# Performance work log

Hardware: AMD Instinct MI355X
Metric: run time of the kernel (lower is better)

## Reference

```python
import math
import jax, jax.numpy as jnp
import numpy as np

B, T, D, S = 4, 8192, 1024, 32  # batch, seq, dim, num_slots; segment L = T // S


def setup_inputs() -> dict:
    key = jax.random.key(0)
    ks = jax.random.split(key, 11)
    d_inv_sqrt = D ** -0.5
    return {
        "x": jax.random.normal(ks[0], (B, T, D), jnp.float32),
        "gate_w": jax.random.normal(ks[1], (D, D), jnp.float32) * d_inv_sqrt,
        "gate_b": jnp.zeros((D,), jnp.float32),
        "read_q_w": jax.random.normal(ks[2], (D, D), jnp.float32) * 0.02,
        "read_k_w": jax.random.normal(ks[3], (D, D), jnp.float32) * 0.02,
        "read_v_w": jax.random.normal(ks[4], (D, D), jnp.float32) * 0.02,
        "output_w": jax.random.normal(ks[5], (D, D), jnp.float32) * d_inv_sqrt,
        "memory_slots": jax.random.normal(ks[6], (S, D), jnp.float32) * 0.02,
        "write_q_w": jax.random.normal(ks[7], (D, D), jnp.float32) * 0.02,
        "write_k_w": jax.random.normal(ks[8], (D, D), jnp.float32) * 0.02,
        "write_v_w": jax.random.normal(ks[9], (D, D), jnp.float32) * 0.02,
    }


def reference(x, gate_w, gate_b, read_q_w, read_k_w, read_v_w, output_w,
              memory_slots, write_q_w, write_k_w, write_v_w):
    b, t, d = x.shape
    s = memory_slots.shape[0]
    L = t // s  # segment length
    scale = 1.0 / math.sqrt(d)

    h = x @ gate_w.T + gate_b  # [B,T,D] gate pre-activation

    # --- write: per-slot attention over that slot's segment (block-diagonal) ---
    q = memory_slots @ write_q_w.T                      # [S,D]
    xs = x.reshape(b, s, L, d)                          # [B,S,L,D]
    k = xs @ write_k_w.T                                # [B,S,L,D]
    v = xs @ write_v_w.T                                # [B,S,L,D]
    wqk = jnp.einsum('sd,bsld->bsl', q, k) * scale      # [B,S,L]
    wattn = jax.nn.softmax(wqk, axis=-1)
    memory = jnp.einsum('bsl,bsld->bsd', wattn, v)      # [B,S,D]

    # --- read: masked cross-attention from tokens to memory slots ---
    rq = x @ read_q_w.T                                 # [B,T,D]
    rk = memory @ read_k_w.T                            # [B,S,D]
    rv = memory @ read_v_w.T                            # [B,S,D]
    rqk = jnp.einsum('btd,bsd->bts', rq, rk) * scale    # [B,T,S]
    seg = jnp.arange(t) // L                            # token -> segment index
    mask = seg[:, None] <= jnp.arange(s)[None, :]       # [T,S]; attend to slots >= own segment
    rqk = jnp.where(mask[None, :, :], rqk, -jnp.inf)
    rattn = jax.nn.softmax(rqk, axis=-1)
    read = jnp.einsum('bts,bsd->btd', rattn, rv)        # [B,T,D]

    y = x + jax.nn.sigmoid(h) * read
    out = y @ output_w.T
    return out, memory
```

## Files before the change

### kernel.cpp

```cpp
#include <hip/hip_runtime.h>
#include <stdint.h>

#define TB 4
#define TT 8192
#define TD 1024
#define TS 32
#define TL 256
#define BT 32768

typedef unsigned short u16;
typedef __bf16 bf16x8 __attribute__((ext_vector_type(8)));
typedef float f32x4 __attribute__((ext_vector_type(4)));

typedef uint32_t u32_g __attribute__((address_space(1)));
typedef uint32_t u32_l __attribute__((address_space(3)));

#define VMWAIT(N) asm volatile("s_waitcnt vmcnt(" #N ")" ::: "memory")
#define LGKM0()   asm volatile("s_waitcnt lgkmcnt(0)" ::: "memory")

__device__ __forceinline__ u16 f2b(float f){
  union { float f; uint32_t u; } a; a.f = f;
  uint32_t r = a.u + 0x7FFFu + ((a.u >> 16) & 1u);
  return (u16)(r >> 16);
}
__device__ __forceinline__ float b2f(u16 u){
  union { uint32_t u; float f; } a; a.u = ((uint32_t)u) << 16;
  return a.f;
}
__device__ __forceinline__ void gll16(const void* g, void* l){
  __builtin_amdgcn_global_load_lds((const u32_g*)g, (u32_l*)l, 16, 0, 0);
}

__global__ void k_tran(const float* __restrict__ w0, const float* __restrict__ w1,
                       const float* __restrict__ w2, const float* __restrict__ w3,
                       const float* __restrict__ w4, const float* __restrict__ ms,
                       u16* __restrict__ t0, u16* __restrict__ t1,
                       u16* __restrict__ t2, u16* __restrict__ t3,
                       u16* __restrict__ t4, u16* __restrict__ msb){
  int tid = threadIdx.x, z = blockIdx.z;
  if (z == 5){
    int i = (blockIdx.y*16 + blockIdx.x)*256 + tid;
    if (i < 8192){
      float4 v = ((const float4*)ms)[i];
      ushort4 u; u.x=f2b(v.x); u.y=f2b(v.y); u.z=f2b(v.z); u.w=f2b(v.w);
      ((ushort4*)msb)[i] = u;
    }
    return;
  }
  const float* src = (z==0)?w0:(z==1)?w1:(z==2)?w2:(z==3)?w3:w4;
  u16* dst = (z==0)?t0:(z==1)?t1:(z==2)?t2:(z==3)?t3:t4;
  __shared__ float sT[64][65];
  int r0 = blockIdx.y*64, c0 = blockIdx.x*64;
  int lr = tid >> 2, lc = (tid & 3)*16;
  #pragma unroll
  for (int j=0; j<4; ++j){
    float4 v = *(const float4*)(src + (size_t)(r0+lr)*TD + c0 + lc + j*4);
    sT[lr][lc+j*4+0]=v.x; sT[lr][lc+j*4+1]=v.y; sT[lr][lc+j*4+2]=v.z; sT[lr][lc+j*4+3]=v.w;
  }
  __syncthreads();
  int oc = tid >> 2, orh = (tid & 3)*16;
  #pragma unroll
  for (int j=0; j<4; ++j){
    ushort4 u;
    u.x = f2b(sT[orh+j*4+0][oc]);
    u.y = f2b(sT[orh+j*4+1][oc]);
    u.z = f2b(sT[orh+j*4+2][oc]);
    u.w = f2b(sT[orh+j*4+3][oc]);
    *(ushort4*)(dst + (size_t)(c0+oc)*TD + r0 + orh + j*4) = u;
  }
}

__global__ __launch_bounds__(512) void k_smmw(
    const u16* __restrict__ A0, const u16* __restrict__ W0, u16* __restrict__ O0, int tr0, float s0,
    const u16* __restrict__ A1, const u16* __restrict__ W1, u16* __restrict__ O1, int tr1, float s1){
  const u16 *A, *W; u16* O; int tr; float sc;
  if (blockIdx.z == 0){ A=A0; W=W0; O=O0; tr=tr0; sc=s0; }
  else                { A=A1; W=W1; O=O1; tr=tr1; sc=s1; }
  int tid = threadIdx.x, lane = tid & 63, wv = tid >> 6;
  int r15 = lane & 15, kg = lane >> 4;
  int wr = wv >> 2, wc = wv & 3;
  int m0 = blockIdx.y*128 + wr*64;
  int n0 = blockIdx.x*128 + wc*32;
  const u16* ap = A + (size_t)(m0 + r15)*TD + kg*8;
  const u16* bp = W + (size_t)(n0 + r15)*TD + kg*8;
  f32x4 acc[4][2];
  #pragma unroll
  for (int i=0;i<4;i++){ f32x4 z={0,0,0,0}; acc[i][0]=z; acc[i][1]=z; }
  #pragma unroll 2
  for (int k0=0; k0<TD; k0+=32){
    bf16x8 b0 = *(const bf16x8*)(bp + k0);
    bf16x8 b1 = *(const bf16x8*)(bp + 16*TD + k0);
    bf16x8 a0 = *(const bf16x8*)(ap + k0);
    bf16x8 a1 = *(const bf16x8*)(ap + 16*TD + k0);
    bf16x8 a2 = *(const bf16x8*)(ap + 32*TD + k0);
    bf16x8 a3 = *(const bf16x8*)(ap + 48*TD + k0);
    acc[0][0] = __builtin_amdgcn_mfma_f32_16x16x32_bf16(a0, b0, acc[0][0], 0,0,0);
    acc[0][1] = __builtin_amdgcn_mfma_f32_16x16x32_bf16(a0, b1, acc[0][1], 0,0,0);
    acc[1][0] = __builtin_amdgcn_mfma_f32_16x16x32_bf16(a1, b0, acc[1][0], 0,0,0);
    acc[1][1] = __builtin_amdgcn_mfma_f32_16x16x32_bf16(a1, b1, acc[1][1], 0,0,0);
    acc[2][0] = __builtin_amdgcn_mfma_f32_16x16x32_bf16(a2, b0, acc[2][0], 0,0,0);
    acc[2][1] = __builtin_amdgcn_mfma_f32_16x16x32_bf16(a2, b1, acc[2][1], 0,0,0);
    acc[3][0] = __builtin_amdgcn_mfma_f32_16x16x32_bf16(a3, b0, acc[3][0], 0,0,0);
    acc[3][1] = __builtin_amdgcn_mfma_f32_16x16x32_bf16(a3, b1, acc[3][1], 0,0,0);
  }
  #pragma unroll
  for (int mf=0; mf<4; ++mf){
    #pragma unroll
    for (int nf=0; nf<2; ++nf){
      int n = n0 + nf*16 + r15;
      #pragma unroll
      for (int qq=0; qq<4; ++qq){
        float v = acc[mf][nf][qq]*sc;
        int m = m0 + mf*16 + kg*4 + qq;
        if (tr) O[(size_t)n*TD + m] = f2b(v);
        else    O[(size_t)m*TD + n] = f2b(v);
      }
    }
  }
}

__global__ __launch_bounds__(512) void k_qk32(const u16* __restrict__ msb, const u16* __restrict__ WzT,
                                              float* __restrict__ qkp){
  int tid = threadIdx.x, lane = tid & 63, wv = tid >> 6;
  int r15 = lane & 15, kg = lane >> 4;
  int n0 = blockIdx.x*128 + wv*16;
  int kbase = blockIdx.y*512;
  const u16* ap = msb + (size_t)r15*TD + kbase + kg*8;
  const u16* bp = WzT + (size_t)(n0 + r15)*TD + kbase + kg*8;
  f32x4 a0 = {0,0,0,0}, a1 = {0,0,0,0};
  #pragma unroll 4
  for (int k0=0; k0<512; k0+=32){
    bf16x8 b  = *(const bf16x8*)(bp + k0);
    bf16x8 x0 = *(const bf16x8*)(ap + k0);
    bf16x8 x1 = *(const bf16x8*)(ap + 16*TD + k0);
    a0 = __builtin_amdgcn_mfma_f32_16x16x32_bf16(x0, b, a0, 0,0,0);
    a1 = __builtin_amdgcn_mfma_f32_16x16x32_bf16(x1, b, a1, 0,0,0);
  }
  const float sc = 1.0f/32.0f;
  float* o = qkp + (size_t)blockIdx.y*32768;
  #pragma unroll
  for (int qq=0; qq<4; ++qq){
    o[(size_t)(kg*4 + qq)*TD + n0 + r15]      = a0[qq]*sc;
    o[(size_t)(16 + kg*4 + qq)*TD + n0 + r15] = a1[qq]*sc;
  }
}

__global__ void k_convdot(const float* __restrict__ x, const float* __restrict__ qkp,
                          u16* __restrict__ xb, float* __restrict__ wqk,
                          const float* __restrict__ s0, const float* __restrict__ s1,
                          const float* __restrict__ s2, const float* __restrict__ s3,
                          const float* __restrict__ s4,
                          u16* __restrict__ d0, u16* __restrict__ d1,
                          u16* __restrict__ d2, u16* __restrict__ d3,
                          u16* __restrict__ d4){
  int tid = threadIdx.x;
  if (blockIdx.x >= 2048){
    int i = (blockIdx.x - 2048)*256 + tid;
    int mi = i >> 18, j = i & 262143;
    const float* src; u16* dst;
    if      (mi == 0){ src = s0; dst = d0; }
    else if (mi == 1){ src = s1; dst = d1; }
    else if (mi == 2){ src = s2; dst = d2; }
    else if (mi == 3){ src = s3; dst = d3; }
    else             { src = s4; dst = d4; }
    float4 v = ((const float4*)src)[j];
    ushort4 u; u.x=f2b(v.x); u.y=f2b(v.y); u.z=f2b(v.z); u.w=f2b(v.w);
    ((ushort4*)dst)[j] = u;
    return;
  }
  int lane = tid & 63, wv = tid >> 6;
  long bt0 = (long)blockIdx.x * 16;
  int sseg = (int)((bt0 & (TT-1)) >> 8);
  float qv[16];
  #pragma unroll
  for (int i=0;i<4;i++){
    const float* qp = qkp + (size_t)sseg*TD + i*256 + lane*4;
    float4 ta = *(const float4*)qp;
    float4 tb = *(const float4*)(qp + 32768);
    qv[i*4+0]=ta.x+tb.x; qv[i*4+1]=ta.y+tb.y; qv[i*4+2]=ta.z+tb.z; qv[i*4+3]=ta.w+tb.w;
  }
  for (int tok = wv; tok < 16; tok += 4){
    long bt = bt0 + tok;
    const float* xr = x + bt*TD;
    float dot = 0.f;
    #pragma unroll
    for (int i=0;i<4;i++){
      float4 t = *(const float4*)(xr + i*256 + lane*4);
      ushort4 u; u.x=f2b(t.x); u.y=f2b(t.y); u.z=f2b(t.z); u.w=f2b(t.w);
      *(ushort4*)(xb + bt*TD + i*256 + lane*4) = u;
      dot += t.x*qv[i*4] + t.y*qv[i*4+1] + t.z*qv[i*4+2] + t.w*qv[i*4+3];
    }
    #pragma unroll
    for (int o=32;o;o>>=1) dot += __shfl_xor(dot, o);
    if (lane == 0) wqk[bt] = dot;
  }
}

__global__ __launch_bounds__(512) void k_wattn_smm(
    const float* __restrict__ wqk, const u16* __restrict__ xb, u16* __restrict__ xbarb,
    const u16* __restrict__ A1, const u16* __restrict__ W1, u16* __restrict__ O1,
    const u16* __restrict__ A2, const u16* __restrict__ W2, u16* __restrict__ O2){
  __shared__ float sw[2][TL];
  __shared__ float red[2][8];
  __shared__ f32x4 part[2][4][64];
  int tid = threadIdx.x;
  if (blockIdx.x < 256){
    int u = tid >> 8;
    int unit = blockIdx.x*2 + u;
    int bs = unit >> 2, dch = unit & 3;
    int b = bs >> 5, s = bs & 31;
    int t2 = tid & 255, lane = t2 & 63, wv = t2 >> 6;
    long base = (long)b*TT + (long)s*TL;
    float v = wqk[base + t2];
    float m = v;
    #pragma unroll
    for (int o=32;o;o>>=1) m = fmaxf(m, __shfl_xor(m, o));
    if (lane == 0) red[u][wv] = m;
    __syncthreads();
    m = fmaxf(fmaxf(red[u][0], red[u][1]), fmaxf(red[u][2], red[u][3]));
    float e = __expf(v - m);
    float sm = e;
    #pragma unroll
    for (int o=32;o;o>>=1) sm += __shfl_xor(sm, o);
    if (lane == 0) red[u][4+wv] = sm;
    __syncthreads();
    sm = red[u][4]+red[u][5]+red[u][6]+red[u][7];
    sw[u][t2] = e / sm;
    __syncthreads();
    int d = dch*256 + lane*4;
    const u16* xp = xb + (base + wv*64)*TD + d;
    f32x4 acc = {0,0,0,0};
    #pragma unroll 8
    for (int i=0; i<64; ++i){
      float w = sw[u][wv*64 + i];
      ushort4 uu = *(const ushort4*)(xp + (size_t)i*TD);
      acc[0] += w*b2f(uu.x); acc[1] += w*b2f(uu.y); acc[2] += w*b2f(uu.z); acc[3] += w*b2f(uu.w);
    }
    part[u][wv][lane] = acc;
    __syncthreads();
    if (wv == 0){
      f32x4 t0 = part[u][0][lane], t1 = part[u][1][lane], t2v = part[u][2][lane], t3 = part[u][3][lane];
      ushort4 o;
      o.x = f2b(t0[0]+t1[0]+t2v[0]+t3[0]);
      o.y = f2b(t0[1]+t1[1]+t2v[1]+t3[1]);
      o.z = f2b(t0[2]+t1[2]+t2v[2]+t3[2]);
      o.w = f2b(t0[3]+t1[3]+t2v[3]+t3[3]);
      *(ushort4*)(xbarb + ((size_t)b*TS + s)*TD + d) = o;
    }
    return;
  }
  int bi = blockIdx.x - 256;
  const u16 *A, *W; u16* O; int tr;
  if (bi < 64){ A=A1; W=W1; O=O1; tr=0; }
  else        { A=A2; W=W2; O=O2; tr=1; bi -= 64; }
  int by = bi >> 3, bx = bi & 7;
  int lane = tid & 63, wv = tid >> 6;
  int r15 = lane & 15, kg = lane >> 4;
  int wr = wv >> 2, wc = wv & 3;
  int m0 = by*128 + wr*64;
  int n0 = bx*128 + wc*32;
  const u16* ap = A + (size_t)(m0 + r15)*TD + kg*8;
  const u16* bp = W + (size_t)(n0 + r15)*TD + kg*8;
  f32x4 acc[4][2];
  #pragma unroll
  for (int i=0;i<4;i++){ f32x4 z={0,0,0,0}; acc[i][0]=z; acc[i][1]=z; }
  #pragma unroll 2
  for (int k0=0; k0<TD; k0+=32){
    bf16x8 b0 = *(const bf16x8*)(bp + k0);
    bf16x8 b1 = *(const bf16x8*)(bp + 16*TD + k0);
    bf16x8 a0 = *(const bf16x8*)(ap + k0);
    bf16x8 a1 = *(const bf16x8*)(ap + 16*TD + k0);
    bf16x8 a2 = *(const bf16x8*)(ap + 32*TD + k0);
    bf16x8 a3 = *(const bf16x8*)(ap + 48*TD + k0);
    acc[0][0] = __builtin_amdgcn_mfma_f32_16x16x32_bf16(a0, b0, acc[0][0], 0,0,0);
    acc[0][1] = __builtin_amdgcn_mfma_f32_16x16x32_bf16(a0, b1, acc[0][1], 0,0,0);
    acc[1][0] = __builtin_amdgcn_mfma_f32_16x16x32_bf16(a1, b0, acc[1][0], 0,0,0);
    acc[1][1] = __builtin_amdgcn_mfma_f32_16x16x32_bf16(a1, b1, acc[1][1], 0,0,0);
    acc[2][0] = __builtin_amdgcn_mfma_f32_16x16x32_bf16(a2, b0, acc[2][0], 0,0,0);
    acc[2][1] = __builtin_amdgcn_mfma_f32_16x16x32_bf16(a2, b1, acc[2][1], 0,0,0);
    acc[3][0] = __builtin_amdgcn_mfma_f32_16x16x32_bf16(a3, b0, acc[3][0], 0,0,0);
    acc[3][1] = __builtin_amdgcn_mfma_f32_16x16x32_bf16(a3, b1, acc[3][1], 0,0,0);
  }
  #pragma unroll
  for (int mf=0; mf<4; ++mf){
    #pragma unroll
    for (int nf=0; nf<2; ++nf){
      int n = n0 + nf*16 + r15;
      #pragma unroll
      for (int qq=0; qq<4; ++qq){
        float v = acc[mf][nf][qq];
        int m = m0 + mf*16 + kg*4 + qq;
        if (tr) O[(size_t)n*TD + m] = f2b(v);
        else    O[(size_t)m*TD + n] = f2b(v);
      }
    }
  }
}

__global__ __launch_bounds__(512) void k_xbar3(const u16* __restrict__ xbarb,
                                               const u16* __restrict__ Wv, const u16* __restrict__ WdT,
                                               const u16* __restrict__ We,
                                               float* __restrict__ memo, u16* __restrict__ rkb,
                                               u16* __restrict__ rvT){
  int z = blockIdx.z;
  const u16* W = (z==0) ? Wv : (z==1) ? WdT : We;
  int tid = threadIdx.x, lane = tid & 63, wv = tid >> 6;
  int r15 = lane & 15, kg = lane >> 4;
  int wr = wv >> 2, wc = wv & 3;
  int n0 = blockIdx.x*128 + wc*32;
  const u16* ap = xbarb + (size_t)(wr*64 + r15)*TD + kg*8;
  const u16* bp = W + (size_t)(n0 + r15)*TD + kg*8;
  f32x4 acc[4][2];
  #pragma unroll
  for (int i=0;i<4;i++){ f32x4 zz={0,0,0,0}; acc[i][0]=zz; acc[i][1]=zz; }
  #pragma unroll 2
  for (int k0=0; k0<TD; k0+=32){
    bf16x8 b0 = *(const bf16x8*)(bp + k0);
    bf16x8 b1 = *(const bf16x8*)(bp + 16*TD + k0);
    bf16x8 a0 = *(const bf16x8*)(ap + k0);
    bf16x8 a1 = *(const bf16x8*)(ap + 16*TD + k0);
    bf16x8 a2 = *(const bf16x8*)(ap + 32*TD + k0);
    bf16x8 a3 = *(const bf16x8*)(ap + 48*TD + k0);
    acc[0][0] = __builtin_amdgcn_mfma_f32_16x16x32_bf16(a0, b0, acc[0][0], 0,0,0);
    acc[0][1] = __builtin_amdgcn_mfma_f32_16x16x32_bf16(a0, b1, acc[0][1], 0,0,0);
    acc[1][0] = __builtin_amdgcn_mfma_f32_16x16x32_bf16(a1, b0, acc[1][0], 0,0,0);
    acc[1][1] = __builtin_amdgcn_mfma_f32_16x16x32_bf16(a1, b1, acc[1][1], 0,0,0);
    acc[2][0] = __builtin_amdgcn_mfma_f32_16x16x32_bf16(a2, b0, acc[2][0], 0,0,0);
    acc[2][1] = __builtin_amdgcn_mfma_f32_16x16x32_bf16(a2, b1, acc[2][1], 0,0,0);
    acc[3][0] = __builtin_amdgcn_mfma_f32_16x16x32_bf16(a3, b0, acc[3][0], 0,0,0);
    acc[3][1] = __builtin_amdgcn_mfma_f32_16x16x32_bf16(a3, b1, acc[3][1], 0,0,0);
  }
  #pragma unroll
  for (int mf=0; mf<4; ++mf){
    #pragma unroll
    for (int nf=0; nf<2; ++nf){
      int n = n0 + nf*16 + r15;
      #pragma unroll
      for (int qq=0; qq<4; ++qq){
        float v = acc[mf][nf][qq];
        int m = wr*64 + mf*16 + kg*4 + qq;
        if (z == 0)      memo[(size_t)m*TD + n] = v;
        else if (z == 1) rkb[(size_t)m*TD + n] = f2b(v);
        else             rvT[((size_t)(m>>5)*TD + n)*TS + (m&31)] = f2b(v);
      }
    }
  }
}

__global__ __launch_bounds__(256) void k_pattn(const u16* __restrict__ xb, const u16* __restrict__ rkb,
                                               u16* __restrict__ P){
  int tid = threadIdx.x, lane = tid & 63, wv = tid >> 6;
  long bt0 = (long)blockIdx.x * 64;
  int b = (int)(bt0 >> 13);
  int smin = (int)((bt0 & (TT-1)) >> 8);
  int r15 = lane & 15, kg = lane >> 4;

  long tw = bt0 + wv*16;
  const u16* ap  = xb  + (size_t)(tw + r15)*TD + kg*8;
  const u16* bp0 = rkb + ((size_t)(b*TS + r15))*TD + kg*8;
  const u16* bp1 = rkb + ((size_t)(b*TS + 16 + r15))*TD + kg*8;
  f32x4 p0 = {0,0,0,0}, p1 = {0,0,0,0};
  #pragma unroll 4
  for (int ks=0; ks<32; ++ks){
    bf16x8 a  = *(const bf16x8*)(ap  + ks*32);
    bf16x8 b0 = *(const bf16x8*)(bp0 + ks*32);
    bf16x8 b1 = *(const bf16x8*)(bp1 + ks*32);
    p0 = __builtin_amdgcn_mfma_f32_16x16x32_bf16(a, b0, p0, 0,0,0);
    p1 = __builtin_amdgcn_mfma_f32_16x16x32_bf16(a, b1, p1, 0,0,0);
  }
  bool msk0 = (r15 < smin), msk1 = (16 + r15 < smin);
  #pragma unroll
  for (int q=0;q<4;q++){
    float l0 = msk0 ? -1e30f : p0[q];
    float l1 = msk1 ? -1e30f : p1[q];
    float mx = fmaxf(l0, l1);
    #pragma unroll
    for (int o=1;o<16;o<<=1) mx = fmaxf(mx, __shfl_xor(mx, o));
    float e0 = msk0 ? 0.f : __expf(l0 - mx);
    float e1 = msk1 ? 0.f : __expf(l1 - mx);
    float smv = e0 + e1;
    #pragma unroll
    for (int o=1;o<16;o<<=1) smv += __shfl_xor(smv, o);
    float rs = 1.f/smv;
    long trow = tw + 4*kg + q;
    P[trow*TS + r15]      = f2b(e0*rs);
    P[trow*TS + 16 + r15] = f2b(e1*rs);
  }
}

template<bool SIG>
__global__ __launch_bounds__(512, 2) void k_gemm(const u16* __restrict__ A, const u16* __restrict__ Bw,
                                                 const float* __restrict__ bias, void* __restrict__ Cp,
                                                 const u16* __restrict__ P, const u16* __restrict__ rvT){
  __shared__ __align__(16) char sL[131072];
  int tid = threadIdx.x, lane = tid & 63, wv = tid >> 6;
  int bid = blockIdx.x;
  int wg = ((bid & 7) << 6) | (bid >> 3);
  int nt = wg & 3, mt = wg >> 2;
  int m0 = mt*256, n0 = nt*256;
  int wr = wv >> 2, wc = wv & 3;
  int r15 = lane & 15, kg = lane >> 4;

  int ard[8], brd[4];
  #pragma unroll
  for (int i=0;i<8;i++){ int row = wr*128 + i*16 + r15; ard[i] = row*128 + ((kg ^ (row&7))<<4); }
  #pragma unroll
  for (int j=0;j<4;j++){ int row = wc*64  + j*16 + r15; brd[j] = row*128 + ((kg ^ (row&7))<<4); }

  const u16* asrc[4]; const u16* bsrc[4]; int ldst[4];
  #pragma unroll
  for (int r=0;r<4;r++){
    int Sp  = r*512 + tid;
    int row = Sp >> 3;
    int kq  = (Sp & 7) ^ (row & 7);
    asrc[r] = A  + (size_t)(m0 + row)*TD + kq*8;
    bsrc[r] = Bw + (size_t)(n0 + row)*TD + kq*8;
    ldst[r] = Sp*16;
  }

  f32x4 acc[8][4];
  #pragma unroll
  for (int i=0;i<8;i++){
    #pragma unroll
    for (int j=0;j<4;j++){ f32x4 z = {0,0,0,0}; acc[i][j] = z; }
  }

  auto stage = [&](int t){
    char* slot = sL + (size_t)(t&1)*65536;
    int k0 = t*64;
    #pragma unroll
    for (int r=0;r<4;r++) gll16(asrc[r] + k0, slot + ldst[r]);
    #pragma unroll
    for (int r=0;r<4;r++) gll16(bsrc[r] + k0, slot + 32768 + ldst[r]);
  };

  auto compute = [&](int t){
    const char* sa = sL + (size_t)(t&1)*65536;
    const char* sb = sa + 32768;
    bf16x8 bfg[4], af[4];
    #pragma unroll
    for (int j=0;j<4;j++) bfg[j] = *(const bf16x8*)(sb + brd[j]);
    #pragma unroll
    for (int i=0;i<4;i++) af[i] = *(const bf16x8*)(sa + ard[i]);
    LGKM0();
    __builtin_amdgcn_sched_barrier(0);
    __builtin_amdgcn_s_setprio(1);
    #pragma unroll
    for (int i=0;i<4;i++){
      #pragma unroll
      for (int j=0;j<4;j++)
        acc[i][j] = __builtin_amdgcn_mfma_f32_16x16x32_bf16(af[i], bfg[j], acc[i][j], 0,0,0);
    }
    __builtin_amdgcn_s_setprio(0);
    bf16x8 af2[4];
    #pragma unroll
    for (int i=0;i<4;i++) af2[i] = *(const bf16x8*)(sa + (ard[4+i]));
    LGKM0();
    __builtin_amdgcn_sched_barrier(0);
    __builtin_amdgcn_s_setprio(1);
    #pragma unroll
    for (int i=0;i<4;i++){
      #pragma unroll
      for (int j=0;j<4;j++)
        acc[4+i][j] = __builtin_amdgcn_mfma_f32_16x16x32_bf16(af2[i], bfg[j], acc[4+i][j], 0,0,0);
    }
    __builtin_amdgcn_s_setprio(0);
    bf16x8 bfh[4], ag[4];
    #pragma unroll
    for (int j=0;j<4;j++) bfh[j] = *(const bf16x8*)(sb + (brd[j]^64));
    #pragma unroll
    for (int i=0;i<4;i++) ag[i] = *(const bf16x8*)(sa + (ard[i]^64));
    LGKM0();
    __builtin_amdgcn_sched_barrier(0);
    __builtin_amdgcn_s_setprio(1);
    #pragma unroll
    for (int i=0;i<4;i++){
      #pragma unroll
      for (int j=0;j<4;j++)
        acc[i][j] = __builtin_amdgcn_mfma_f32_16x16x32_bf16(ag[i], bfh[j], acc[i][j], 0,0,0);
    }
    __builtin_amdgcn_s_setprio(0);
    bf16x8 ag2[4];
    #pragma unroll
    for (int i=0;i<4;i++) ag2[i] = *(const bf16x8*)(sa + (ard[4+i]^64));
    LGKM0();
    __builtin_amdgcn_sched_barrier(0);
    __builtin_amdgcn_s_setprio(1);
    #pragma unroll
    for (int i=0;i<4;i++){
      #pragma unroll
      for (int j=0;j<4;j++)
        acc[4+i][j] = __builtin_amdgcn_mfma_f32_16x16x32_bf16(ag2[i], bfh[j], acc[4+i][j], 0,0,0);
    }
    __builtin_amdgcn_s_setprio(0);
  };

  stage(0);
  for (int t=0; t<16; ++t){
    if (t > 0) __builtin_amdgcn_s_barrier();
    if (t < 15){
      stage(t+1);
      VMWAIT(8);
    } else {
      VMWAIT(0);
    }
    __builtin_amdgcn_s_barrier();
    compute(t);
  }

  if (SIG){
    int b = m0 >> 13;
    bf16x8 vfrag[4];
    #pragma unroll
    for (int j=0;j<4;j++){
      int n = n0 + wc*64 + j*16 + r15;
      vfrag[j] = *(const bf16x8*)(rvT + ((size_t)b*TD + n)*TS + kg*8);
    }
    #pragma unroll
    for (int i=0;i<8;i++){
      int tokbase = m0 + wr*128 + i*16;
      bf16x8 pfrag = *(const bf16x8*)(P + (size_t)(tokbase + r15)*TS + kg*8);
      f32x4 rd[4];
      #pragma unroll
      for (int j=0;j<4;j++){
        f32x4 z = {0,0,0,0};
        rd[j] = __builtin_amdgcn_mfma_f32_16x16x32_bf16(pfrag, vfrag[j], z, 0,0,0);
      }
      int mrow = tokbase + kg*4;
      #pragma unroll
      for (int j=0;j<4;j++){
        int n = n0 + wc*64 + j*16 + r15;
        float bj = bias[n];
        #pragma unroll
        for (int q=0;q<4;q++){
          float g = 1.f/(1.f + __expf(-(acc[i][j][q] + bj)));
          size_t idx = (size_t)(mrow + q)*TD + n;
          float xv = b2f(A[idx]);
          ((u16*)Cp)[idx] = f2b(xv + g*rd[j][q]);
        }
      }
    }
  } else {
    #pragma unroll
    for (int i=0;i<8;i++){
      int mrow = m0 + wr*128 + i*16 + kg*4;
      #pragma unroll
      for (int j=0;j<4;j++){
        int n = n0 + wc*64 + j*16 + r15;
        #pragma unroll
        for (int q=0;q<4;q++){
          size_t idx = (size_t)(mrow + q)*TD + n;
          ((float*)Cp)[idx] = acc[i][j][q];
        }
      }
    }
  }
}

extern "C" void kernel_launch(void* const* d_in, const int* in_sizes, int n_in,
                              void* d_out, int out_size, void* d_ws, size_t ws_size,
                              hipStream_t stream){
  const float* x   = (const float*)d_in[0];
  const float* gw  = (const float*)d_in[1];
  const float* gb  = (const float*)d_in[2];
  const float* rqw = (const float*)d_in[3];
  const float* rkw = (const float*)d_in[4];
  const float* rvw = (const float*)d_in[5];
  const float* ow  = (const float*)d_in[6];
  const float* ms  = (const float*)d_in[7];
  const float* wqw = (const float*)d_in[8];
  const float* wkw = (const float*)d_in[9];
  const float* wvw = (const float*)d_in[10];
  float* out = (float*)d_out;
  float* mem_out = out + (size_t)BT*TD;

  char* o = (char*)d_out;
  u16* xb    = (u16*)o;
  u16* Pb    = (u16*)(o + 67108864);
  u16* gwb   = (u16*)(o + 69206016);
  u16* wvwb  = (u16*)(o + 71303168);
  u16* rkwb  = (u16*)(o + 73400320);
  u16* rvwb  = (u16*)(o + 75497472);
  u16* xbarb = (u16*)(o + 79757312);
  u16* rvT   = (u16*)(o + 80281600);
  u16* WvT   = (u16*)(o + 84934656);
  u16* WrqT  = (u16*)(o + 87031808);
  u16* WqT   = (u16*)(o + 89128960);
  u16* WkT   = (u16*)(o + 91226112);
  u16* We    = (u16*)(o + 95420416);
  u16* WdT   = (u16*)(o + 97517568);
  u16* WzT   = (u16*)(o + 99614720);
  u16* msb   = (u16*)(o + 101711872);
  u16* WrkT  = (u16*)(o + 103809024);
  u16* WgT   = (u16*)(o + 105906176);

  char* w = (char*)d_ws;
  u16*   gy    = (u16*)(w);
  float* wqkb  = (float*)(w + 67108864);
  float* qkp   = (float*)(w + 67239936);
  u16*   rkb   = (u16*)(w + 67502080);
  u16*   owb   = (u16*)(w + 68288512);

  k_tran<<<dim3(16,16,6),256,0,stream>>>(wvw, rqw, wqw, wkw, rkw, ms,
                                         WvT, WrqT, WqT, WkT, WrkT, msb);
  k_smmw<<<dim3(8,8,2),512,0,stream>>>(WqT, WkT, WzT, 1, 1.f,
                                       WrkT, WrqT, WgT, 1, 1.f/32.f);
  k_qk32<<<dim3(8,2),512,0,stream>>>(msb, WzT, qkp);
  k_convdot<<<7168,256,0,stream>>>(x, qkp, xb, wqkb,
                                   gw, ow, wvw, rkw, rvw,
                                   gwb, owb, wvwb, rkwb, rvwb);
  k_wattn_smm<<<384,512,0,stream>>>(wqkb, xb, xbarb,
                                    rvwb, WvT, We,
                                    WvT, WgT, WdT);
  k_xbar3<<<dim3(8,1,3),512,0,stream>>>(xbarb, wvwb, WdT, We, mem_out, rkb, rvT);
  k_pattn<<<512,256,0,stream>>>(xb, rkb, Pb);
  k_gemm<true><<<512,512,0,stream>>>(xb, gwb, gb, gy, Pb, rvT);
  k_gemm<false><<<512,512,0,stream>>>(gy, owb, nullptr, d_out, nullptr, nullptr);
}
```

Baseline: 396.1 us.

## Reassociate write-query product to skip the D×D weight-weight GEMM

The code now computes q = memory_slots @ Wq^T directly, fused into the transpose kernel with on-the-fly bf16 conversion, and then qk = q @ Wk. This replaces forming the full WzT = Wq·Wk product followed by a split-K qk32 kernel. That removes a 1024³ GEMM and one kernel launch, and also drops the Wq transpose and memory-slot conversion. The xbar3 kernel is also retiled to narrower N tiles with twice as many blocks, and some loops are unrolled by 4. The tradeoff is a small single-row-of-blocks GEMM now sitting in the transpose kernel, plus an extra bf16 rounding of q.

```diff
diff --git a/kernel.cpp b/kernel.cpp
--- a/kernel.cpp
+++ b/kernel.cpp
@@ -30,25 +30,46 @@
 __device__ __forceinline__ void gll16(const void* g, void* l){
   __builtin_amdgcn_global_load_lds((const u32_g*)g, (u32_l*)l, 16, 0, 0);
 }
+__device__ __forceinline__ bf16x8 cvt8(const float* p){
+  float4 a = *(const float4*)p, b = *(const float4*)(p+4);
+  union { u16 s[8]; bf16x8 v; } u;
+  u.s[0]=f2b(a.x); u.s[1]=f2b(a.y); u.s[2]=f2b(a.z); u.s[3]=f2b(a.w);
+  u.s[4]=f2b(b.x); u.s[5]=f2b(b.y); u.s[6]=f2b(b.z); u.s[7]=f2b(b.w);
+  return u.v;
+}
 
 __global__ void k_tran(const float* __restrict__ w0, const float* __restrict__ w1,
                        const float* __restrict__ w2, const float* __restrict__ w3,
-                       const float* __restrict__ w4, const float* __restrict__ ms,
+                       const float* __restrict__ ms, const float* __restrict__ Wq,
                        u16* __restrict__ t0, u16* __restrict__ t1,
                        u16* __restrict__ t2, u16* __restrict__ t3,
-                       u16* __restrict__ t4, u16* __restrict__ msb){
+                       u16* __restrict__ qb){
   int tid = threadIdx.x, z = blockIdx.z;
-  if (z == 5){
-    int i = (blockIdx.y*16 + blockIdx.x)*256 + tid;
-    if (i < 8192){
-      float4 v = ((const float4*)ms)[i];
-      ushort4 u; u.x=f2b(v.x); u.y=f2b(v.y); u.z=f2b(v.z); u.w=f2b(v.w);
-      ((ushort4*)msb)[i] = u;
+  if (z == 4){
+    if (blockIdx.y != 0) return;
+    int lane = tid & 63, wv = tid >> 6;
+    int r15 = lane & 15, kg = lane >> 4;
+    int n0 = blockIdx.x*64 + wv*16;
+    const float* ap = ms + (size_t)r15*TD + kg*8;
+    const float* bp = Wq + (size_t)(n0 + r15)*TD + kg*8;
+    f32x4 a0 = {0,0,0,0}, a1 = {0,0,0,0};
+    #pragma unroll 4
+    for (int k0=0; k0<TD; k0+=32){
+      bf16x8 b  = cvt8(bp + k0);
+      bf16x8 x0 = cvt8(ap + k0);
+      bf16x8 x1 = cvt8(ap + 16*TD + k0);
+      a0 = __builtin_amdgcn_mfma_f32_16x16x32_bf16(x0, b, a0, 0,0,0);
+      a1 = __builtin_amdgcn_mfma_f32_16x16x32_bf16(x1, b, a1, 0,0,0);
+    }
+    #pragma unroll
+    for (int qq=0; qq<4; ++qq){
+      qb[(size_t)(kg*4 + qq)*TD + n0 + r15]      = f2b(a0[qq]);
+      qb[(size_t)(16 + kg*4 + qq)*TD + n0 + r15] = f2b(a1[qq]);
     }
     return;
   }
-  const float* src = (z==0)?w0:(z==1)?w1:(z==2)?w2:(z==3)?w3:w4;
-  u16* dst = (z==0)?t0:(z==1)?t1:(z==2)?t2:(z==3)?t3:t4;
+  const float* src = (z==0)?w0:(z==1)?w1:(z==2)?w2:w3;
+  u16* dst = (z==0)?t0:(z==1)?t1:(z==2)?t2:t3;
   __shared__ float sT[64][65];
   int r0 = blockIdx.y*64, c0 = blockIdx.x*64;
   int lr = tid >> 2, lc = (tid & 3)*16;
@@ -70,23 +91,42 @@
   }
 }
 
-__global__ __launch_bounds__(512) void k_smmw(
-    const u16* __restrict__ A0, const u16* __restrict__ W0, u16* __restrict__ O0, int tr0, float s0,
-    const u16* __restrict__ A1, const u16* __restrict__ W1, u16* __restrict__ O1, int tr1, float s1){
-  const u16 *A, *W; u16* O; int tr; float sc;
-  if (blockIdx.z == 0){ A=A0; W=W0; O=O0; tr=tr0; sc=s0; }
-  else                { A=A1; W=W1; O=O1; tr=tr1; sc=s1; }
+__global__ __launch_bounds__(512) void k_smmw2(
+    const u16* __restrict__ WrkT, const u16* __restrict__ WrqT, u16* __restrict__ WgT,
+    const u16* __restrict__ qb, const u16* __restrict__ WkT, float* __restrict__ qkp){
   int tid = threadIdx.x, lane = tid & 63, wv = tid >> 6;
   int r15 = lane & 15, kg = lane >> 4;
+  if (blockIdx.z == 1){
+    if (blockIdx.y != 0) return;
+    int n0 = blockIdx.x*128 + wv*16;
+    const u16* ap = qb + (size_t)r15*TD + kg*8;
+    const u16* bp = WkT + (size_t)(n0 + r15)*TD + kg*8;
+    f32x4 a0 = {0,0,0,0}, a1 = {0,0,0,0};
+    #pragma unroll 4
+    for (int k0=0; k0<TD; k0+=32){
+      bf16x8 b  = *(const bf16x8*)(bp + k0);
+      bf16x8 x0 = *(const bf16x8*)(ap + k0);
+      bf16x8 x1 = *(const bf16x8*)(ap + 16*TD + k0);
+      a0 = __builtin_amdgcn_mfma_f32_16x16x32_bf16(x0, b, a0, 0,0,0);
+      a1 = __builtin_amdgcn_mfma_f32_16x16x32_bf16(x1, b, a1, 0,0,0);
+    }
+    const float sc = 1.0f/32.0f;
+    #pragma unroll
+    for (int qq=0; qq<4; ++qq){
+      qkp[(size_t)(kg*4 + qq)*TD + n0 + r15]      = a0[qq]*sc;
+      qkp[(size_t)(16 + kg*4 + qq)*TD + n0 + r15] = a1[qq]*sc;
+    }
+    return;
+  }
   int wr = wv >> 2, wc = wv & 3;
   int m0 = blockIdx.y*128 + wr*64;
   int n0 = blockIdx.x*128 + wc*32;
-  const u16* ap = A + (size_t)(m0 + r15)*TD + kg*8;
-  const u16* bp = W + (size_t)(n0 + r15)*TD + kg*8;
+  const u16* ap = WrkT + (size_t)(m0 + r15)*TD + kg*8;
+  const u16* bp = WrqT + (size_t)(n0 + r15)*TD + kg*8;
   f32x4 acc[4][2];
   #pragma unroll
   for (int i=0;i<4;i++){ f32x4 z={0,0,0,0}; acc[i][0]=z; acc[i][1]=z; }
-  #pragma unroll 2
+  #pragma unroll 4
   for (int k0=0; k0<TD; k0+=32){
     bf16x8 b0 = *(const bf16x8*)(bp + k0);
     bf16x8 b1 = *(const bf16x8*)(bp + 16*TD + k0);
@@ -103,6 +143,7 @@
     acc[3][0] = __builtin_amdgcn_mfma_f32_16x16x32_bf16(a3, b0, acc[3][0], 0,0,0);
     acc[3][1] = __builtin_amdgcn_mfma_f32_16x16x32_bf16(a3, b1, acc[3][1], 0,0,0);
   }
+  const float sc = 1.0f/32.0f;
   #pragma unroll
   for (int mf=0; mf<4; ++mf){
     #pragma unroll
@@ -112,36 +153,9 @@
       for (int qq=0; qq<4; ++qq){
         float v = acc[mf][nf][qq]*sc;
         int m = m0 + mf*16 + kg*4 + qq;
-        if (tr) O[(size_t)n*TD + m] = f2b(v);
-        else    O[(size_t)m*TD + n] = f2b(v);
+        WgT[(size_t)n*TD + m] = f2b(v);
       }
     }
-  }
-}
-
-__global__ __launch_bounds__(512) void k_qk32(const u16* __restrict__ msb, const u16* __restrict__ WzT,
-                                              float* __restrict__ qkp){
-  int tid = threadIdx.x, lane = tid & 63, wv = tid >> 6;
-  int r15 = lane & 15, kg = lane >> 4;
-  int n0 = blockIdx.x*128 + wv*16;
-  int kbase = blockIdx.y*512;
-  const u16* ap = msb + (size_t)r15*TD + kbase + kg*8;
-  const u16* bp = WzT + (size_t)(n0 + r15)*TD + kbase + kg*8;
-  f32x4 a0 = {0,0,0,0}, a1 = {0,0,0,0};
-  #pragma unroll 4
-  for (int k0=0; k0<512; k0+=32){
-    bf16x8 b  = *(const bf16x8*)(bp + k0);
-    bf16x8 x0 = *(const bf16x8*)(ap + k0);
-    bf16x8 x1 = *(const bf16x8*)(ap + 16*TD + k0);
-    a0 = __builtin_amdgcn_mfma_f32_16x16x32_bf16(x0, b, a0, 0,0,0);
-    a1 = __builtin_amdgcn_mfma_f32_16x16x32_bf16(x1, b, a1, 0,0,0);
-  }
-  const float sc = 1.0f/32.0f;
-  float* o = qkp + (size_t)blockIdx.y*32768;
-  #pragma unroll
-  for (int qq=0; qq<4; ++qq){
-    o[(size_t)(kg*4 + qq)*TD + n0 + r15]      = a0[qq]*sc;
-    o[(size_t)(16 + kg*4 + qq)*TD + n0 + r15] = a1[qq]*sc;
   }
 }
 
@@ -174,10 +188,8 @@
   float qv[16];
   #pragma unroll
   for (int i=0;i<4;i++){
-    const float* qp = qkp + (size_t)sseg*TD + i*256 + lane*4;
-    float4 ta = *(const float4*)qp;
-    float4 tb = *(const float4*)(qp + 32768);
-    qv[i*4+0]=ta.x+tb.x; qv[i*4+1]=ta.y+tb.y; qv[i*4+2]=ta.z+tb.z; qv[i*4+3]=ta.w+tb.w;
+    float4 ta = *(const float4*)(qkp + (size_t)sseg*TD + i*256 + lane*4);
+    qv[i*4+0]=ta.x; qv[i*4+1]=ta.y; qv[i*4+2]=ta.z; qv[i*4+3]=ta.w;
   }
   for (int tok = wv; tok < 16; tok += 4){
     long bt = bt0 + tok;
@@ -264,7 +276,7 @@
   f32x4 acc[4][2];
   #pragma unroll
   for (int i=0;i<4;i++){ f32x4 z={0,0,0,0}; acc[i][0]=z; acc[i][1]=z; }
-  #pragma unroll 2
+  #pragma unroll 4
   for (int k0=0; k0<TD; k0+=32){
     bf16x8 b0 = *(const bf16x8*)(bp + k0);
     bf16x8 b1 = *(const bf16x8*)(bp + 16*TD + k0);
@@ -307,42 +319,34 @@
   int tid = threadIdx.x, lane = tid & 63, wv = tid >> 6;
   int r15 = lane & 15, kg = lane >> 4;
   int wr = wv >> 2, wc = wv & 3;
-  int n0 = blockIdx.x*128 + wc*32;
+  int n0 = blockIdx.x*64 + wc*16;
   const u16* ap = xbarb + (size_t)(wr*64 + r15)*TD + kg*8;
   const u16* bp = W + (size_t)(n0 + r15)*TD + kg*8;
-  f32x4 acc[4][2];
-  #pragma unroll
-  for (int i=0;i<4;i++){ f32x4 zz={0,0,0,0}; acc[i][0]=zz; acc[i][1]=zz; }
-  #pragma unroll 2
+  f32x4 acc[4];
+  #pragma unroll
+  for (int i=0;i<4;i++){ f32x4 zz={0,0,0,0}; acc[i]=zz; }
+  #pragma unroll 4
   for (int k0=0; k0<TD; k0+=32){
     bf16x8 b0 = *(const bf16x8*)(bp + k0);
-    bf16x8 b1 = *(const bf16x8*)(bp + 16*TD + k0);
     bf16x8 a0 = *(const bf16x8*)(ap + k0);
     bf16x8 a1 = *(const bf16x8*)(ap + 16*TD + k0);
     bf16x8 a2 = *(const bf16x8*)(ap + 32*TD + k0);
     bf16x8 a3 = *(const bf16x8*)(ap + 48*TD + k0);
-    acc[0][0] = __builtin_amdgcn_mfma_f32_16x16x32_bf16(a0, b0, acc[0][0], 0,0,0);
-    acc[0][1] = __builtin_amdgcn_mfma_f32_16x16x32_bf16(a0, b1, acc[0][1], 0,0,0);
-    acc[1][0] = __builtin_amdgcn_mfma_f32_16x16x32_bf16(a1, b0, acc[1][0], 0,0,0);
-    acc[1][1] = __builtin_amdgcn_mfma_f32_16x16x32_bf16(a1, b1, acc[1][1], 0,0,0);
-    acc[2][0] = __builtin_amdgcn_mfma_f32_16x16x32_bf16(a2, b0, acc[2][0], 0,0,0);
-    acc[2][1] = __builtin_amdgcn_mfma_f32_16x16x32_bf16(a2, b1, acc[2][1], 0,0,0);
-    acc[3][0] = __builtin_amdgcn_mfma_f32_16x16x32_bf16(a3, b0, acc[3][0], 0,0,0);
-    acc[3][1] = __builtin_amdgcn_mfma_f32_16x16x32_bf16(a3, b1, acc[3][1], 0,0,0);
+    acc[0] = __builtin_amdgcn_mfma_f32_16x16x32_bf16(a0, b0, acc[0], 0,0,0);
+    acc[1] = __builtin_amdgcn_mfma_f32_16x16x32_bf16(a1, b0, acc[1], 0,0,0);
+    acc[2] = __builtin_amdgcn_mfma_f32_16x16x32_bf16(a2, b0, acc[2], 0,0,0);
+    acc[3] = __builtin_amdgcn_mfma_f32_16x16x32_bf16(a3, b0, acc[3], 0,0,0);
   }
   #pragma unroll
   for (int mf=0; mf<4; ++mf){
-    #pragma unroll
-    for (int nf=0; nf<2; ++nf){
-      int n = n0 + nf*16 + r15;
-      #pragma unroll
-      for (int qq=0; qq<4; ++qq){
-        float v = acc[mf][nf][qq];
-        int m = wr*64 + mf*16 + kg*4 + qq;
-        if (z == 0)      memo[(size_t)m*TD + n] = v;
-        else if (z == 1) rkb[(size_t)m*TD + n] = f2b(v);
-        else             rvT[((size_t)(m>>5)*TD + n)*TS + (m&31)] = f2b(v);
-      }
+    int n = n0 + r15;
+    #pragma unroll
+    for (int qq=0; qq<4; ++qq){
+      float v = acc[mf][qq];
+      int m = wr*64 + mf*16 + kg*4 + qq;
+      if (z == 0)      memo[(size_t)m*TD + n] = v;
+      else if (z == 1) rkb[(size_t)m*TD + n] = f2b(v);
+      else             rvT[((size_t)(m>>5)*TD + n)*TS + (m&31)] = f2b(v);
     }
   }
 }
@@ -585,12 +589,10 @@
   u16* rvT   = (u16*)(o + 80281600);
   u16* WvT   = (u16*)(o + 84934656);
   u16* WrqT  = (u16*)(o + 87031808);
-  u16* WqT   = (u16*)(o + 89128960);
+  u16* qbb   = (u16*)(o + 89128960);
   u16* WkT   = (u16*)(o + 91226112);
   u16* We    = (u16*)(o + 95420416);
   u16* WdT   = (u16*)(o + 97517568);
-  u16* WzT   = (u16*)(o + 99614720);
-  u16* msb   = (u16*)(o + 101711872);
   u16* WrkT  = (u16*)(o + 103809024);
   u16* WgT   = (u16*)(o + 105906176);
 
@@ -601,18 +603,16 @@
   u16*   rkb   = (u16*)(w + 67502080);
   u16*   owb   = (u16*)(w + 68288512);
 
-  k_tran<<<dim3(16,16,6),256,0,stream>>>(wvw, rqw, wqw, wkw, rkw, ms,
-                                         WvT, WrqT, WqT, WkT, WrkT, msb);
-  k_smmw<<<dim3(8,8,2),512,0,stream>>>(WqT, WkT, WzT, 1, 1.f,
-                                       WrkT, WrqT, WgT, 1, 1.f/32.f);
-  k_qk32<<<dim3(8,2),512,0,stream>>>(msb, WzT, qkp);
+  k_tran<<<dim3(16,16,5),256,0,stream>>>(wvw, rqw, wkw, rkw, ms, wqw,
+                                         WvT, WrqT, WkT, WrkT, qbb);
+  k_smmw2<<<dim3(8,8,2),512,0,stream>>>(WrkT, WrqT, WgT, qbb, WkT, qkp);
   k_convdot<<<7168,256,0,stream>>>(x, qkp, xb, wqkb,
                                    gw, ow, wvw, rkw, rvw,
                                    gwb, owb, wvwb, rkwb, rvwb);
   k_wattn_smm<<<384,512,0,stream>>>(wqkb, xb, xbarb,
                                     rvwb, WvT, We,
                                     WvT, WgT, WdT);
-  k_xbar3<<<dim3(8,1,3),512,0,stream>>>(xbarb, wvwb, WdT, We, mem_out, rkb, rvT);
+  k_xbar3<<<dim3(16,1,3),512,0,stream>>>(xbarb, wvwb, WdT, We, mem_out, rkb, rvT);
   k_pattn<<<512,256,0,stream>>>(xb, rkb, Pb);
   k_gemm<true><<<512,512,0,stream>>>(xb, gwb, gb, gy, Pb, rvT);
   k_gemm<false><<<512,512,0,stream>>>(gy, owb, nullptr, d_out, nullptr, nullptr);
```

Result: no change. 401.2 us (+1.3%).
